# Kernel tuning notes

Hardware: AMD Instinct MI355X
Metric: run time of the kernel (lower is better)

The kernel has to match this reference:

```python
import jax, jax.numpy as jnp
import numpy as np

B, T, D, H = 16, 2048, 512, 512  # batch, seq_len, input_dim, hidden_dim


def setup_inputs() -> dict:
    key = jax.random.key(0)
    k1, k2, k3 = jax.random.split(key, 3)
    x = jax.random.normal(k1, (B, T, D), dtype=jnp.float32)
    # vanilla tanh RnnCell parameters
    W_xh = jax.random.normal(k2, (D, H), dtype=jnp.float32) / np.float32(np.sqrt(D))
    W_hh = jax.random.normal(k3, (H, H), dtype=jnp.float32) / np.float32(np.sqrt(H))
    b = jnp.zeros((H,), dtype=jnp.float32)
    # DFA feedback matrix, 'diagonal' init branch: diag(linspace(0,1,H))
    A = jnp.diag(jnp.linspace(0.0, 1.0, H).astype(jnp.float32))
    return {"x": x, "W_xh": W_xh, "W_hh": W_hh, "b": b, "A": A}


def reference(x, W_xh, W_hh, b, A):
    # Forward of DfaRnn: sequential RNN loop. detach() does not change forward
    # values, so this is a plain tanh RNN scan. A only affects the backward.
    Bb = x.shape[0]
    h0 = jnp.zeros((Bb, W_hh.shape[0]), dtype=x.dtype)

    def step(h, xt):
        h_new = jnp.tanh(xt @ W_xh + h @ W_hh + b)
        return h_new, h_new

    _, hs = jax.lax.scan(step, h0, jnp.swapaxes(x, 0, 1))  # [T,B,H]
    return jnp.swapaxes(hs, 0, 1)  # [B,T,H]
```

## Files before the change

kernel.cpp:

```cpp
#include <hip/hip_runtime.h>
#include <cmath>

#define B_ 16
#define T_ 2048
#define D_ 512
#define H_ 512

__global__ __launch_bounds__(256) void gemm_xw(
    const float* __restrict__ x,
    const float* __restrict__ Wxh,
    const float* __restrict__ bias,
    float* __restrict__ out)
{
    const int tid = threadIdx.x;
    const int m0 = blockIdx.y * 64;
    const int n0 = blockIdx.x * 64;

    __shared__ float As[16][68];
    __shared__ float Bs[16][68];

    const int tx = tid & 15, ty = tid >> 4;
    float acc[4][4] = {};

    const int arow = tid >> 2;
    const int akq  = (tid & 3) * 4;
    const int brow = tid >> 4;
    const int bcol = (tid & 15) * 4;

    for (int k0 = 0; k0 < D_; k0 += 16) {
        float4 a4 = *(const float4*)(x + (size_t)(m0 + arow) * D_ + k0 + akq);
        float4 b4 = *(const float4*)(Wxh + (size_t)(k0 + brow) * H_ + n0 + bcol);
        __syncthreads();
        As[akq + 0][arow] = a4.x;
        As[akq + 1][arow] = a4.y;
        As[akq + 2][arow] = a4.z;
        As[akq + 3][arow] = a4.w;
        *(float4*)(&Bs[brow][bcol]) = b4;
        __syncthreads();
#pragma unroll
        for (int kk = 0; kk < 16; ++kk) {
            float4 av = *(const float4*)(&As[kk][ty * 4]);
            float4 bv = *(const float4*)(&Bs[kk][tx * 4]);
            float a_[4] = {av.x, av.y, av.z, av.w};
            float b_[4] = {bv.x, bv.y, bv.z, bv.w};
#pragma unroll
            for (int i = 0; i < 4; ++i)
#pragma unroll
                for (int j = 0; j < 4; ++j) acc[i][j] += a_[i] * b_[j];
        }
    }

    const float4 bv = *(const float4*)(bias + n0 + tx * 4);
#pragma unroll
    for (int i = 0; i < 4; ++i) {
        const int m = m0 + ty * 4 + i;
        float4 o;
        o.x = acc[i][0] + bv.x;
        o.y = acc[i][1] + bv.y;
        o.z = acc[i][2] + bv.z;
        o.w = acc[i][3] + bv.w;
        *(float4*)(out + (size_t)m * H_ + n0 + tx * 4) = o;
    }
}

__global__ __launch_bounds__(512) void rnn_rec(
    const float* __restrict__ Whh,
    float* __restrict__ out,
    unsigned long long* __restrict__ ws)
{
    const int tid = threadIdx.x;
    const int b = blockIdx.x & 15;
    const int s = blockIdx.x >> 4;
    const int j = tid & 63;
    const int p = tid >> 6;
    const int col = (s << 6) + j;

    __shared__ float h_lds[H_];
    __shared__ float part[8 * 64];

    float W_reg[64];
#pragma unroll
    for (int r = 0; r < 64; ++r)
        W_reg[r] = Whh[(size_t)(p * 64 + r) * H_ + col];

    h_lds[tid] = 0.0f;
    __syncthreads();

    float* outb = out + (size_t)b * T_ * H_;
    unsigned long long* wsb = ws + (size_t)b * 2 * H_;

    float xw0 = 0.0f, xw1 = 0.0f;
    if (p == 0) {
        xw0 = outb[(size_t)0 * H_ + col];
        xw1 = outb[(size_t)1 * H_ + col];
    }

    for (int t = 0; t < T_; ++t) {
        float acc = 0.0f;
        const float4* hv = (const float4*)(h_lds + (p << 6));
#pragma unroll
        for (int i = 0; i < 16; ++i) {
            float4 h4 = hv[i];
            acc += h4.x * W_reg[4 * i + 0];
            acc += h4.y * W_reg[4 * i + 1];
            acc += h4.z * W_reg[4 * i + 2];
            acc += h4.w * W_reg[4 * i + 3];
        }
        part[tid] = acc;
        __syncthreads();

        const unsigned int tag = (unsigned int)(t + 1);
        const int slot = (t + 1) & 1;
        unsigned long long* wslot = wsb + (size_t)slot * H_;

        if (p == 0) {
            float ssum = xw0;
#pragma unroll
            for (int q = 0; q < 8; ++q) ssum += part[q * 64 + j];
            union { unsigned int u; float f; } cv;
            cv.f = tanhf(ssum);
            unsigned long long pv =
                ((unsigned long long)tag << 32) | (unsigned long long)cv.u;
            __hip_atomic_store(wslot + col, pv, __ATOMIC_RELAXED,
                               __HIP_MEMORY_SCOPE_AGENT);
            outb[(size_t)t * H_ + col] = cv.f;
            h_lds[col] = cv.f;
            xw0 = xw1;
            xw1 = (t + 2 < T_) ? outb[(size_t)(t + 2) * H_ + col] : 0.0f;
        } else {
            const int q = (p == s) ? 0 : p;
            unsigned long long* src = wslot + (q << 6) + j;
            unsigned long long v;
            do {
                v = __hip_atomic_load(src, __ATOMIC_RELAXED,
                                      __HIP_MEMORY_SCOPE_AGENT);
            } while ((unsigned int)(v >> 32) < tag);
            union { unsigned int u; float f; } cv;
            cv.u = (unsigned int)v;
            h_lds[(q << 6) + j] = cv.f;
        }
        __syncthreads();
    }
}

extern "C" void kernel_launch(void* const* d_in, const int* in_sizes, int n_in,
                              void* d_out, int out_size, void* d_ws,
                              size_t ws_size, hipStream_t stream) {
    const float* x    = (const float*)d_in[0];
    const float* Wxh  = (const float*)d_in[1];
    const float* Whh  = (const float*)d_in[2];
    const float* bias = (const float*)d_in[3];
    float* out = (float*)d_out;

    hipMemsetAsync(d_ws, 0, (size_t)B_ * 2 * H_ * sizeof(unsigned long long),
                   stream);

    dim3 ggrid(H_ / 64, (B_ * T_) / 64, 1);
    gemm_xw<<<ggrid, 256, 0, stream>>>(x, Wxh, bias, out);

    rnn_rec<<<128, 512, 0, stream>>>(Whh, out, (unsigned long long*)d_ws);
}
```

Before: 3.075 ms.

## Use sc0 fast-path flag exchange with fallback, and enlarge GEMM tiles to 128x128

The recurrent kernel now publishes each hidden value twice: once through a raw global store with the sc0 cache modifier, and once through the original agent-scope atomic slot. Consumers spin on the fast copy with a bounded count and fall back permanently to the atomic path if it does not arrive, aiming to cut the per-step cross-block synchronisation latency. Separately, the input-projection GEMM moves from 64x64 tiles with 4x4 per thread to 128x128 tiles with 8x8 per thread, for more register reuse. The extra store per step adds traffic, the workspace doubles, and the sc0 visibility semantics across CUs are the main correctness risk.

```diff
diff --git a/kernel.cpp b/kernel.cpp
--- a/kernel.cpp
+++ b/kernel.cpp
@@ -13,21 +13,21 @@
     float* __restrict__ out)
 {
     const int tid = threadIdx.x;
-    const int m0 = blockIdx.y * 64;
-    const int n0 = blockIdx.x * 64;
+    const int n0 = blockIdx.x * 128;
+    const int m0 = blockIdx.y * 128;
 
-    __shared__ float As[16][68];
-    __shared__ float Bs[16][68];
+    __shared__ float As[8][132];
+    __shared__ float Bs[8][132];
 
     const int tx = tid & 15, ty = tid >> 4;
-    float acc[4][4] = {};
+    float acc[8][8] = {};
 
-    const int arow = tid >> 2;
-    const int akq  = (tid & 3) * 4;
-    const int brow = tid >> 4;
-    const int bcol = (tid & 15) * 4;
+    const int arow = tid >> 1;
+    const int akq  = (tid & 1) * 4;
+    const int brow = tid >> 5;
+    const int bcol = (tid & 31) * 4;
 
-    for (int k0 = 0; k0 < D_; k0 += 16) {
+    for (int k0 = 0; k0 < D_; k0 += 8) {
         float4 a4 = *(const float4*)(x + (size_t)(m0 + arow) * D_ + k0 + akq);
         float4 b4 = *(const float4*)(Wxh + (size_t)(k0 + brow) * H_ + n0 + bcol);
         __syncthreads();
@@ -38,30 +38,37 @@
         *(float4*)(&Bs[brow][bcol]) = b4;
         __syncthreads();
 #pragma unroll
-        for (int kk = 0; kk < 16; ++kk) {
-            float4 av = *(const float4*)(&As[kk][ty * 4]);
-            float4 bv = *(const float4*)(&Bs[kk][tx * 4]);
-            float a_[4] = {av.x, av.y, av.z, av.w};
-            float b_[4] = {bv.x, bv.y, bv.z, bv.w};
+        for (int kk = 0; kk < 8; ++kk) {
+            float4 a0 = *(const float4*)(&As[kk][ty * 8]);
+            float4 a1 = *(const float4*)(&As[kk][ty * 8 + 4]);
+            float4 b0 = *(const float4*)(&Bs[kk][tx * 8]);
+            float4 b1 = *(const float4*)(&Bs[kk][tx * 8 + 4]);
+            float a_[8] = {a0.x, a0.y, a0.z, a0.w, a1.x, a1.y, a1.z, a1.w};
+            float b_[8] = {b0.x, b0.y, b0.z, b0.w, b1.x, b1.y, b1.z, b1.w};
 #pragma unroll
-            for (int i = 0; i < 4; ++i)
+            for (int i = 0; i < 8; ++i)
 #pragma unroll
-                for (int j = 0; j < 4; ++j) acc[i][j] += a_[i] * b_[j];
+                for (int j = 0; j < 8; ++j) acc[i][j] += a_[i] * b_[j];
         }
     }
 
-    const float4 bv = *(const float4*)(bias + n0 + tx * 4);
+    const float4 bv0 = *(const float4*)(bias + n0 + tx * 8);
+    const float4 bv1 = *(const float4*)(bias + n0 + tx * 8 + 4);
+    const float bb[8] = {bv0.x, bv0.y, bv0.z, bv0.w, bv1.x, bv1.y, bv1.z, bv1.w};
 #pragma unroll
-    for (int i = 0; i < 4; ++i) {
-        const int m = m0 + ty * 4 + i;
-        float4 o;
-        o.x = acc[i][0] + bv.x;
-        o.y = acc[i][1] + bv.y;
-        o.z = acc[i][2] + bv.z;
-        o.w = acc[i][3] + bv.w;
-        *(float4*)(out + (size_t)m * H_ + n0 + tx * 4) = o;
+    for (int i = 0; i < 8; ++i) {
+        const int m = m0 + ty * 8 + i;
+        float4 o0, o1;
+        o0.x = acc[i][0] + bb[0]; o0.y = acc[i][1] + bb[1];
+        o0.z = acc[i][2] + bb[2]; o0.w = acc[i][3] + bb[3];
+        o1.x = acc[i][4] + bb[4]; o1.y = acc[i][5] + bb[5];
+        o1.z = acc[i][6] + bb[6]; o1.w = acc[i][7] + bb[7];
+        *(float4*)(out + (size_t)m * H_ + n0 + tx * 8)     = o0;
+        *(float4*)(out + (size_t)m * H_ + n0 + tx * 8 + 4) = o1;
     }
 }
+
+#define FAST_SPIN 20000
 
 __global__ __launch_bounds__(512) void rnn_rec(
     const float* __restrict__ Whh,
@@ -87,13 +94,16 @@
     __syncthreads();
 
     float* outb = out + (size_t)b * T_ * H_;
-    unsigned long long* wsb = ws + (size_t)b * 2 * H_;
+    unsigned long long* fastb = ws + (size_t)b * 2 * H_;
+    unsigned long long* slowb = ws + (size_t)B_ * 2 * H_ + (size_t)b * 2 * H_;
 
     float xw0 = 0.0f, xw1 = 0.0f;
     if (p == 0) {
         xw0 = outb[(size_t)0 * H_ + col];
         xw1 = outb[(size_t)1 * H_ + col];
     }
+
+    bool use_fast = true;
 
     for (int t = 0; t < T_; ++t) {
         float acc = 0.0f;
@@ -111,7 +121,7 @@
 
         const unsigned int tag = (unsigned int)(t + 1);
         const int slot = (t + 1) & 1;
-        unsigned long long* wslot = wsb + (size_t)slot * H_;
+        const size_t base = (size_t)slot * H_;
 
         if (p == 0) {
             float ssum = xw0;
@@ -121,7 +131,10 @@
             cv.f = tanhf(ssum);
             unsigned long long pv =
                 ((unsigned long long)tag << 32) | (unsigned long long)cv.u;
-            __hip_atomic_store(wslot + col, pv, __ATOMIC_RELAXED,
+            unsigned long long* fdst = fastb + base + col;
+            asm volatile("global_store_dwordx2 %0, %1, off sc0"
+                         :: "v"(fdst), "v"(pv) : "memory");
+            __hip_atomic_store(slowb + base + col, pv, __ATOMIC_RELAXED,
                                __HIP_MEMORY_SCOPE_AGENT);
             outb[(size_t)t * H_ + col] = cv.f;
             h_lds[col] = cv.f;
@@ -129,12 +142,27 @@
             xw1 = (t + 2 < T_) ? outb[(size_t)(t + 2) * H_ + col] : 0.0f;
         } else {
             const int q = (p == s) ? 0 : p;
-            unsigned long long* src = wslot + (q << 6) + j;
-            unsigned long long v;
-            do {
-                v = __hip_atomic_load(src, __ATOMIC_RELAXED,
-                                      __HIP_MEMORY_SCOPE_AGENT);
-            } while ((unsigned int)(v >> 32) < tag);
+            const size_t idx = base + (q << 6) + j;
+            unsigned long long v = 0;
+            if (use_fast) {
+                unsigned long long* fsrc = fastb + idx;
+                int spins = FAST_SPIN;
+                for (;;) {
+                    asm volatile(
+                        "global_load_dwordx2 %0, %1, off sc0\n\t"
+                        "s_waitcnt vmcnt(0)"
+                        : "=v"(v) : "v"(fsrc) : "memory");
+                    if ((unsigned int)(v >> 32) >= tag) break;
+                    if (--spins == 0) { use_fast = false; break; }
+                }
+            }
+            if (!use_fast) {
+                unsigned long long* ssrc = slowb + idx;
+                do {
+                    v = __hip_atomic_load(ssrc, __ATOMIC_RELAXED,
+                                          __HIP_MEMORY_SCOPE_AGENT);
+                } while ((unsigned int)(v >> 32) < tag);
+            }
             union { unsigned int u; float f; } cv;
             cv.u = (unsigned int)v;
             h_lds[(q << 6) + j] = cv.f;
@@ -152,10 +180,11 @@
     const float* bias = (const float*)d_in[3];
     float* out = (float*)d_out;
 
-    hipMemsetAsync(d_ws, 0, (size_t)B_ * 2 * H_ * sizeof(unsigned long long),
+    hipMemsetAsync(d_ws, 0,
+                   (size_t)2 * B_ * 2 * H_ * sizeof(unsigned long long),
                    stream);
 
-    dim3 ggrid(H_ / 64, (B_ * T_) / 64, 1);
+    dim3 ggrid(H_ / 128, (B_ * T_) / 128, 1);
     gemm_xw<<<ggrid, 256, 0, stream>>>(x, Wxh, bias, out);
 
     rnn_rec<<<128, 512, 0, stream>>>(Whh, out, (unsigned long long*)d_ws);
```

Measured after the change: 9.788 ms. 218% more time.
